# Optimization experiments

Hardware: AMD Instinct MI355X
Metric: run time of the kernel (lower is better)

Reference implementation:

```python
import math
import jax, jax.numpy as jnp
import numpy as np

INV_SQRT_2_PI = math.pow(2.0 * math.pi, -0.5)

N_POINTS = 4_194_304
COMPONENTS = 128
MZ_MIN = 0.0
MZ_MAX = 1.0


def setup_inputs() -> dict:
    key = jax.random.key(0)
    k_mz, k_noise = jax.random.split(key)
    # evaluation points in the domain [mz_min, mz_max]
    mz = jax.random.uniform(k_mz, (N_POINTS,), dtype=jnp.float32,
                            minval=MZ_MIN, maxval=MZ_MAX)
    # parameter init mirrors GMM1D.__init__
    std_dev = 0.5 * (MZ_MAX - MZ_MIN) / COMPONENTS
    means = jnp.linspace(MZ_MIN, MZ_MAX, COMPONENTS, dtype=jnp.float32)
    noise = 0.5 * std_dev * jax.random.normal(k_noise, (COMPONENTS,), dtype=jnp.float32)
    mu = means + noise
    lv = jnp.full((COMPONENTS,), 2.0 * math.log(std_dev), dtype=jnp.float32)
    pi_l = jnp.zeros((COMPONENTS,), dtype=jnp.float32)
    return {"mz": mz, "pi_l": pi_l, "mu": mu, "lv": lv}


def reference(mz, pi_l, mu, lv):
    """GMM1D.prob: prob[n] = sum_k softmax(pi_l)_k * N(mz[n]; mu_k, exp(lv_k))"""
    pi = jax.nn.softmax(pi_l, axis=0)                      # [K]
    inv_var = jnp.exp(-lv)                                 # [K] = 1/sigma^2
    coef = pi * (INV_SQRT_2_PI * jnp.exp(-0.5 * lv))       # [K] pi_k / (sqrt(2pi) sigma_k)
    diff = mz[:, None] - mu[None, :]                       # [N, K]
    dens = jnp.exp(-0.5 * diff * diff * inv_var[None, :])  # [N, K] unnormalized gaussian
    prob = jnp.einsum('nk,k->n', dens, coef)               # [N]
    return prob
```

## Files before the change

kernel.cpp:

```cpp
#include <hip/hip_runtime.h>
#include <math.h>

#define K_COMP 128
#define LOG2E 1.4426950408889634f
#define INV_SQRT_2PI 0.3989422804014327f
#define PPT 16
#define BLOCK 256
#define WRAD 5
#define WWIN 12

__global__ __launch_bounds__(BLOCK) void gmm_fused(const float* __restrict__ mz,
                                                   const float* __restrict__ pi_l,
                                                   const float* __restrict__ mu,
                                                   const float* __restrict__ lv,
                                                   float* __restrict__ out,
                                                   int n) {
    __shared__ float2 sp2[K_COMP];
    __shared__ float4 sp4[K_COMP];
    __shared__ float sA;
    __shared__ int sWin;

    int tid = threadIdx.x;

    if (tid < 64) {
        int t = tid;
        float p0 = pi_l[t];
        float p1 = pi_l[t + 64];
        float m = fmaxf(p0, p1);
        #pragma unroll
        for (int off = 1; off < 64; off <<= 1)
            m = fmaxf(m, __shfl_xor(m, off, 64));
        float e0 = expf(p0 - m);
        float e1 = expf(p1 - m);
        float s = e0 + e1;
        #pragma unroll
        for (int off = 1; off < 64; off <<= 1)
            s += __shfl_xor(s, off, 64);
        float inv_s = 1.0f / s;

        float rad = 0.0f, amin = 1e30f, amax = -1e30f;
        #pragma unroll
        for (int j = 0; j < 2; j++) {
            int k = t + 64 * j;
            float e = (j == 0) ? e0 : e1;
            float pi_k = e * inv_s;
            float lvk = lv[k];
            float A = -0.5f * expf(-lvk) * LOG2E;
            float coef = pi_k * INV_SQRT_2PI * expf(-0.5f * lvk);
            float lc = log2f(coef);
            float muk = mu[k];
            sp4[k] = make_float4(muk, A, lc, 0.0f);
            sp2[k] = make_float2(muk, lc);
            float num = fmaxf(lc + 30.0f, 0.0f);
            float dk = sqrtf(num / (-A));
            float r = fabsf(muk * 127.0f - (float)k) + dk * 127.0f;
            rad = fmaxf(rad, r);
            amin = fminf(amin, A);
            amax = fmaxf(amax, A);
        }
        #pragma unroll
        for (int off = 1; off < 64; off <<= 1) {
            rad = fmaxf(rad, __shfl_xor(rad, off, 64));
            amin = fminf(amin, __shfl_xor(amin, off, 64));
            amax = fmaxf(amax, __shfl_xor(amax, off, 64));
        }
        if (t == 0) {
            sA = amax;
            sWin = (amin == amax && rad + 0.5f <= (float)WRAD) ? 1 : 0;
        }
    }
    __syncthreads();

    const float A = sA;
    const int win = sWin;
    long blockBase = (long)blockIdx.x * (BLOCK * PPT);

    float x[PPT];
    #pragma unroll
    for (int p = 0; p < PPT; p++) {
        long idx = blockBase + (long)p * BLOCK + tid;
        x[p] = (idx < n) ? mz[idx] : 0.0f;
    }

    float acc[PPT];
    if (win) {
        #pragma unroll
        for (int p = 0; p < PPT; p++) {
            float xp = x[p];
            int kc = (int)fmaf(xp, 127.0f, 0.5f);
            int k0 = min(max(kc - WRAD, 0), K_COMP - WWIN);
            float a = 0.0f;
            #pragma unroll
            for (int j = 0; j < WWIN; j++) {
                float2 pr = sp2[k0 + j];
                float d = xp - pr.x;
                float t = __builtin_fmaf(d * A, d, pr.y);
                a += __builtin_amdgcn_exp2f(t);
            }
            acc[p] = a;
        }
    } else {
        #pragma unroll
        for (int p = 0; p < PPT; p++) acc[p] = 0.0f;
        for (int k = 0; k < K_COMP; k++) {
            float4 pr = sp4[k];
            #pragma unroll
            for (int p = 0; p < PPT; p++) {
                float d = x[p] - pr.x;
                float t = __builtin_fmaf(d * pr.y, d, pr.z);
                acc[p] += __builtin_amdgcn_exp2f(t);
            }
        }
    }

    #pragma unroll
    for (int p = 0; p < PPT; p++) {
        long idx = blockBase + (long)p * BLOCK + tid;
        if (idx < n) out[idx] = acc[p];
    }
}

extern "C" void kernel_launch(void* const* d_in, const int* in_sizes, int n_in,
                              void* d_out, int out_size, void* d_ws, size_t ws_size,
                              hipStream_t stream) {
    const float* mz   = (const float*)d_in[0];
    const float* pi_l = (const float*)d_in[1];
    const float* mu   = (const float*)d_in[2];
    const float* lv   = (const float*)d_in[3];
    float* out = (float*)d_out;
    int n = in_sizes[0];

    int grid = (n + BLOCK * PPT - 1) / (BLOCK * PPT);
    gmm_fused<<<grid, BLOCK, 0, stream>>>(mz, pi_l, mu, lv, out, n);
}
```

Measured before the change: 90.75 us.

## Replicate per-component parameters across LDS banks to avoid gather bank conflicts

```diff
diff --git a/kernel.cpp b/kernel.cpp
--- a/kernel.cpp
+++ b/kernel.cpp
@@ -8,6 +8,8 @@
 #define BLOCK 256
 #define WRAD 5
 #define WWIN 12
+#define REP 32
+#define ROW 64
 
 __global__ __launch_bounds__(BLOCK) void gmm_fused(const float* __restrict__ mz,
                                                    const float* __restrict__ pi_l,
@@ -15,9 +17,10 @@
                                                    const float* __restrict__ lv,
                                                    float* __restrict__ out,
                                                    int n) {
-    __shared__ float2 sp2[K_COMP];
-    __shared__ float4 sp4[K_COMP];
-    __shared__ float sA;
+    __shared__ float sp[K_COMP * ROW];
+    __shared__ float4 sRaw[K_COMP];
+    __shared__ float sAk[K_COMP];
+    __shared__ float sAs;
     __shared__ int sWin;
 
     int tid = threadIdx.x;
@@ -49,8 +52,7 @@
             float coef = pi_k * INV_SQRT_2PI * expf(-0.5f * lvk);
             float lc = log2f(coef);
             float muk = mu[k];
-            sp4[k] = make_float4(muk, A, lc, 0.0f);
-            sp2[k] = make_float2(muk, lc);
+            sRaw[k] = make_float4(muk, A, lc, 0.0f);
             float num = fmaxf(lc + 30.0f, 0.0f);
             float dk = sqrtf(num / (-A));
             float r = fabsf(muk * 127.0f - (float)k) + dk * 127.0f;
@@ -65,14 +67,28 @@
             amax = fmaxf(amax, __shfl_xor(amax, off, 64));
         }
         if (t == 0) {
-            sA = amax;
+            sAs = amax;
             sWin = (amin == amax && rad + 0.5f <= (float)WRAD) ? 1 : 0;
         }
     }
     __syncthreads();
 
-    const float A = sA;
+    {
+        int k = tid >> 1;
+        int half = tid & 1;
+        float4 r = sRaw[k];
+        float v = half ? r.z : r.x;
+        float4 vv = make_float4(v, v, v, v);
+        float4* dst = (float4*)&sp[k * ROW + half * REP];
+        #pragma unroll
+        for (int i = 0; i < 8; i++) dst[i] = vv;
+        if (!half) sAk[k] = r.y;
+    }
+    __syncthreads();
+
+    const float A = sAs;
     const int win = sWin;
+    const int lrep = tid & (REP - 1);
     long blockBase = (long)blockIdx.x * (BLOCK * PPT);
 
     float x[PPT];
@@ -87,14 +103,20 @@
         #pragma unroll
         for (int p = 0; p < PPT; p++) {
             float xp = x[p];
-            int kc = (int)fmaf(xp, 127.0f, 0.5f);
+            int kc = (int)__builtin_fmaf(xp, 127.0f, 0.5f);
             int k0 = min(max(kc - WRAD, 0), K_COMP - WWIN);
+            const float* row = &sp[(k0 << 6) + lrep];
+            float mv[WWIN], cv[WWIN];
+            #pragma unroll
+            for (int j = 0; j < WWIN; j++) {
+                mv[j] = row[j * ROW];
+                cv[j] = row[j * ROW + REP];
+            }
             float a = 0.0f;
             #pragma unroll
             for (int j = 0; j < WWIN; j++) {
-                float2 pr = sp2[k0 + j];
-                float d = xp - pr.x;
-                float t = __builtin_fmaf(d * A, d, pr.y);
+                float d = xp - mv[j];
+                float t = __builtin_fmaf(d * A, d, cv[j]);
                 a += __builtin_amdgcn_exp2f(t);
             }
             acc[p] = a;
@@ -103,11 +125,13 @@
         #pragma unroll
         for (int p = 0; p < PPT; p++) acc[p] = 0.0f;
         for (int k = 0; k < K_COMP; k++) {
-            float4 pr = sp4[k];
+            float mk = sp[(k << 6) + lrep];
+            float ck = sp[(k << 6) + REP + lrep];
+            float Ak = sAk[k];
             #pragma unroll
             for (int p = 0; p < PPT; p++) {
-                float d = x[p] - pr.x;
-                float t = __builtin_fmaf(d * pr.y, d, pr.z);
+                float d = x[p] - mk;
+                float t = __builtin_fmaf(d * Ak, d, ck);
                 acc[p] += __builtin_amdgcn_exp2f(t);
             }
         }
```

After: 86.85 us. -4.3%, faster.
